# Performance work log

Measured on AMD Instinct MI355X. Metric: run time of the kernel, lower is better.

Reference implementation:

```python
import jax, jax.numpy as jnp
import numpy as np

TAU = 0.1
LAM = 1.0
LOG_NOISE = 1e-12
COS_EPS = 1e-8      # torch CosineSimilarity eps
NORM_EPS = 1e-12    # torch F.normalize eps


def setup_inputs() -> dict:
    key = jax.random.key(0)
    k1, k2, k3, k4 = jax.random.split(key, 4)
    B, D, S = 8192, 128, 64
    z1s = jax.random.normal(k1, (B, D), dtype=jnp.float32)
    z2s = jax.random.normal(k2, (B, D), dtype=jnp.float32)
    z1_c_outs = jax.random.uniform(k3, (B, S), dtype=jnp.float32)
    z1_subject_labels = jax.random.normal(k4, (B, S), dtype=jnp.float32)
    return {"z1s": z1s, "z2s": z2s, "z1_c_outs": z1_c_outs,
            "z1_subject_labels": z1_subject_labels}


def _l2_normalize(x, eps):
    # normalize rows; clamp norm from below like torch
    n = jnp.linalg.norm(x, axis=1, keepdims=True)
    return x / jnp.maximum(n, eps)


def reference(z1s, z2s, z1_c_outs, z1_subject_labels):
    B = z1s.shape[0]
    z1 = z1s.reshape(B, -1)
    z2 = z2s.reshape(B, -1)
    n1 = _l2_normalize(z1, COS_EPS)
    n2 = _l2_normalize(z2, COS_EPS)

    # all-pairs cosine similarities, scaled by temperature
    S12 = jnp.matmul(n1, n2.T) / TAU   # [B, B] sim(z1_i, z2_k)/tau
    S11 = jnp.matmul(n1, n1.T) / TAU   # [B, B] sim(z1_i, z1_k)/tau

    e12 = jnp.exp(S12)
    e11 = jnp.exp(S11)
    numerator = jnp.diagonal(e12)                       # exp(sim(z1_i, z2_i)/tau)
    # denom_i = sum_k e12[i,k] + sum_{k != i} e11[i,k]
    denom = e12.sum(axis=1) + e11.sum(axis=1) - jnp.diagonal(e11)
    contrastive = -jnp.log(LOG_NOISE + numerator / denom)
    loss = contrastive.sum() / (B * (2.0 * B - 1.0))

    # adversarial term: -lam * log(1 - normalized_pred[i, argmax(label_i)])
    c = _l2_normalize(z1_c_outs, NORM_EPS)
    j = jnp.argmax(z1_subject_labels, axis=1)           # [B] int
    picked = c[jnp.arange(B), j]
    loss = loss + LAM * (-jnp.log(LOG_NOISE + 1.0 - picked)).sum()
    return loss
```

## Files before the change

kernel.cpp:

```cpp
#include <hip/hip_runtime.h>
#include <hip/hip_bf16.h>
#include <math.h>


#define NROWS 8192
#define DFEAT 128

typedef __bf16 bf16_t;
typedef __bf16 bf16x8 __attribute__((ext_vector_type(8)));
typedef __bf16 bf16x2 __attribute__((ext_vector_type(2)));
typedef float  f32x4  __attribute__((ext_vector_type(4)));

__device__ __forceinline__ float fexp2(float x) {
#if __has_builtin(__builtin_amdgcn_exp2f)
  return __builtin_amdgcn_exp2f(x);
#else
  return exp2f(x);
#endif
}

__device__ __forceinline__ void stage16(const void* gsrc, void* ldst) {
  __builtin_amdgcn_global_load_lds(
      (const __attribute__((address_space(1))) unsigned int*)gsrc,
      (__attribute__((address_space(3))) unsigned int*)ldst, 16, 0, 0);
}

__global__ __launch_bounds__(256)
void sa_prep_kernel(const float* __restrict__ z1,
                    const float* __restrict__ z2,
                    bf16_t* __restrict__ Abuf,
                    bf16_t* __restrict__ Kc,
                    float* __restrict__ numv,
                    float* __restrict__ d11v) {
  __shared__ __align__(16) bf16_t L[3][16][136];

  int wave = threadIdx.x >> 6;
  int lane = threadIdx.x & 63;
  int tile = blockIdx.x;

  const float SCL = 14.426950408889634f;

#pragma unroll
  for (int r = 0; r < 4; ++r) {
    int rl  = wave * 4 + r;
    int row = tile * 16 + rl;

    float2 a = ((const float2*)(z1 + (size_t)row * DFEAT))[lane];
    float2 b = ((const float2*)(z2 + (size_t)row * DFEAT))[lane];

    float s1  = a.x * a.x + a.y * a.y;
    float s2  = b.x * b.x + b.y * b.y;
    float s12 = a.x * b.x + a.y * b.y;
#pragma unroll
    for (int m = 32; m; m >>= 1) {
      s1  += __shfl_xor(s1, m, 64);
      s2  += __shfl_xor(s2, m, 64);
      s12 += __shfl_xor(s12, m, 64);
    }
    float r1 = 1.0f / fmaxf(sqrtf(s1), 1e-8f);
    float r2 = 1.0f / fmaxf(sqrtf(s2), 1e-8f);

    bf16x2 av;  av[0] = (bf16_t)(a.x * r1 * SCL); av[1] = (bf16_t)(a.y * r1 * SCL);
    bf16x2 k2v; k2v[0] = (bf16_t)(b.x * r2);      k2v[1] = (bf16_t)(b.y * r2);
    bf16x2 k1v; k1v[0] = (bf16_t)(a.x * r1);      k1v[1] = (bf16_t)(a.y * r1);

    *(bf16x2*)&L[0][rl][2 * lane] = av;
    *(bf16x2*)&L[1][rl][2 * lane] = k2v;
    *(bf16x2*)&L[2][rl][2 * lane] = k1v;

    if (lane == 0) {
      numv[row] = expf(10.0f * s12 * r1 * r2);
      d11v[row] = expf(10.0f * s1 * r1 * r1);
    }
  }
  __syncthreads();

#pragma unroll
  for (int sel = 0; sel < 3; ++sel) {
    int u   = threadIdx.x;
    int kf  = u >> 6;
    int qk  = (u >> 4) & 3;
    int r16 = u & 15;
    bf16x8 v = *(const bf16x8*)&L[sel][r16][kf * 32 + qk * 8];
    bf16_t* dst = (sel == 0) ? (Abuf + (size_t)tile * 2048)
                : (sel == 1) ? (Kc + (size_t)tile * 2048)
                             : (Kc + (size_t)(512 + tile) * 2048);
    *(bf16x8*)(dst + u * 8) = v;
  }
}

__global__ __launch_bounds__(512, 4)
void sa_main_kernel(const bf16_t* __restrict__ Abuf,
                    const bf16_t* __restrict__ Kc,
                    float* __restrict__ T2t) {
  __shared__ __align__(16) bf16_t bsm[32768];

  int wave = threadIdx.x >> 6;
  int lane = threadIdx.x & 63;
  int quad = lane >> 4;

  int id     = blockIdx.x;
  int xcd    = id & 7;
  int within = id >> 3;
  int by     = xcd * 8 + (within >> 4);
  int bx     = within & 15;
  int rowBase = bx * 512 + wave * 64;

  const bf16x8* ap = (const bf16x8*)Abuf + (size_t)(rowBase >> 4) * 256 + lane;
  bf16x8 afrag[4][4];
#pragma unroll
  for (int s = 0; s < 4; ++s)
#pragma unroll
    for (int kfi = 0; kfi < 4; ++kfi)
      afrag[s][kfi] = ap[(s * 4 + kfi) * 64];

  const char* src = (const char*)Kc + (size_t)by * 65536 +
                    (size_t)wave * 8192 + (size_t)lane * 16;
  char* dst = (char*)&bsm[0] + wave * 8192;
#pragma unroll
  for (int i = 0; i < 8; ++i) stage16(src + i * 1024, dst + i * 1024);

  __syncthreads();

  f32x4 sums[4];
#pragma unroll
  for (int s = 0; s < 4; ++s) sums[s] = (f32x4){0.f, 0.f, 0.f, 0.f};

#pragma unroll 1
  for (int i = 0; i < 8; ++i) {
    int p = (wave + i) & 7;
    const bf16_t* base = &bsm[0] + p * 4096;
#pragma unroll
    for (int tt = 0; tt < 2; ++tt) {
      const bf16x8* bs = (const bf16x8*)(base + tt * 2048);
      bf16x8 bfr[4];
#pragma unroll
      for (int kfi = 0; kfi < 4; ++kfi) bfr[kfi] = bs[kfi * 64 + lane];
#pragma unroll
      for (int s = 0; s < 4; ++s) {
        f32x4 c = {0.f, 0.f, 0.f, 0.f};
        __builtin_amdgcn_s_setprio(1);
#pragma unroll
        for (int kfi = 0; kfi < 4; ++kfi)
          c = __builtin_amdgcn_mfma_f32_16x16x32_bf16(afrag[s][kfi], bfr[kfi],
                                                      c, 0, 0, 0);
        __builtin_amdgcn_s_setprio(0);
#pragma unroll
        for (int r = 0; r < 4; ++r) sums[s][r] += fexp2(c[r]);
      }
    }
  }

  int l15 = lane & 15;
#pragma unroll
  for (int s = 0; s < 4; ++s) {
    f32x4 st;
#pragma unroll
    for (int r = 0; r < 4; ++r) {
      float v = sums[s][r];
      v += __shfl_xor(v, 1, 64);
      v += __shfl_xor(v, 2, 64);
      v += __shfl_xor(v, 4, 64);
      v += __shfl_xor(v, 8, 64);
      st[r] = v;
    }
    if (l15 == 0)
      *(f32x4*)(T2t + (size_t)by * 8192 + rowBase + s * 16 + quad * 4) = st;
  }
}

__global__ __launch_bounds__(256)
void sa_final_adv_kernel(const float* __restrict__ T2t,
                         const float* __restrict__ numv,
                         const float* __restrict__ d11v,
                         const float* __restrict__ c,
                         const float* __restrict__ lab,
                         float* __restrict__ partial) {
  int wave = threadIdx.x >> 6;
  int lane = threadIdx.x & 63;

  float acc = 0.0f;
#pragma unroll
  for (int i = 0; i < 4; ++i) {
    int row = blockIdx.x * 16 + wave * 4 + i;

    float cv = c[row * 64 + lane];
    float lv = lab[row * 64 + lane];
    float tv = T2t[(size_t)lane * 8192 + row];

    float ss = cv * cv;
    float bestv = lv;
    int   besti = lane;
#pragma unroll
    for (int m = 32; m; m >>= 1) {
      ss += __shfl_xor(ss, m, 64);
      tv += __shfl_xor(tv, m, 64);
      float ov = __shfl_xor(bestv, m, 64);
      int   oi = __shfl_xor(besti, m, 64);
      if (ov > bestv || (ov == bestv && oi < besti)) { bestv = ov; besti = oi; }
    }
    float picked = __shfl(cv, besti, 64) / fmaxf(sqrtf(ss), 1e-12f);

    if (lane == 0) {
      float denom = tv - d11v[row];
      acc += -logf(1e-12f + numv[row] / denom) * (1.0f / 134209536.0f)
             - logf(1e-12f + 1.0f - picked);
    }
  }

  __shared__ float wacc[4];
  if (lane == 0) wacc[wave] = acc;
  __syncthreads();
  if (threadIdx.x == 0)
    partial[blockIdx.x] = wacc[0] + wacc[1] + wacc[2] + wacc[3];
}

__global__ __launch_bounds__(256)
void sa_reduce_kernel(const float* __restrict__ partial,
                      float* __restrict__ out) {
  float v = partial[threadIdx.x] + partial[threadIdx.x + 256];
#pragma unroll
  for (int m = 32; m; m >>= 1) v += __shfl_xor(v, m, 64);
  __shared__ float wacc[4];
  if ((threadIdx.x & 63) == 0) wacc[threadIdx.x >> 6] = v;
  __syncthreads();
  if (threadIdx.x == 0) out[0] = wacc[0] + wacc[1] + wacc[2] + wacc[3];
}

extern "C" void kernel_launch(void* const* d_in, const int* in_sizes, int n_in,
                              void* d_out, int out_size, void* d_ws,
                              size_t ws_size, hipStream_t stream) {
  const float* z1  = (const float*)d_in[0];
  const float* z2  = (const float*)d_in[1];
  const float* co  = (const float*)d_in[2];
  const float* lab = (const float*)d_in[3];
  float* out = (float*)d_out;

  char* ws = (char*)d_ws;
  bf16_t* Abuf  = (bf16_t*)ws;
  bf16_t* Kc    = (bf16_t*)(ws + 2u * 1024 * 1024);
  float*  T2t   = (float*)(ws + 6u * 1024 * 1024);
  float*  numv  = (float*)(ws + 8u * 1024 * 1024);
  float*  d11v  = numv + NROWS;
  float*  part  = d11v + NROWS;

  sa_prep_kernel<<<NROWS / 16, 256, 0, stream>>>(z1, z2, Abuf, Kc, numv,
                                                 d11v);
  sa_main_kernel<<<1024, 512, 0, stream>>>(Abuf, Kc, T2t);
  sa_final_adv_kernel<<<NROWS / 16, 256, 0, stream>>>(T2t, numv, d11v, co,
                                                      lab, part);
  sa_reduce_kernel<<<1, 256, 0, stream>>>(part, out);
}
```

Measured before the change: 108.1 us.

## Exploit symmetry of self-similarity matrix to skip half of e11 tiles

The main kernel now computes only the lower-triangular blocks of the symmetric z1·z1ᵀ exp matrix. Each such block's column sums are accumulated in shared memory and written out as the row sums of the mirrored block, which cuts the grid from 1024 to 784 blocks. This removes roughly a quarter of the MFMA and exp work, at the cost of extra shuffles, LDS accumulation, a barrier and a serial triangle-index search per block.

```diff
diff --git a/kernel.cpp b/kernel.cpp
--- a/kernel.cpp
+++ b/kernel.cpp
@@ -94,17 +94,30 @@
                     const bf16_t* __restrict__ Kc,
                     float* __restrict__ T2t) {
   __shared__ __align__(16) bf16_t bsm[32768];
+  __shared__ float colred[8][256];
 
   int wave = threadIdx.x >> 6;
   int lane = threadIdx.x & 63;
   int quad = lane >> 4;
 
-  int id     = blockIdx.x;
-  int xcd    = id & 7;
-  int within = id >> 3;
-  int by     = xcd * 8 + (within >> 4);
-  int bx     = within & 15;
-  int rowBase = bx * 512 + wave * 64;
+  int id  = blockIdx.x;
+  int swz = (id & 7) * 98 + (id >> 3);
+
+  int I, J, chunk;
+  bool e11;
+  if (swz < 512) {
+    I = swz >> 5; J = swz & 31; chunk = J; e11 = false;
+  } else {
+    int m = swz - 512;
+    I = 0;
+    while ((I + 1) * (I + 2) <= m) ++I;
+    J = m - I * (I + 1);
+    chunk = 32 + J; e11 = true;
+  }
+
+  int rowBase = I * 512 + wave * 64;
+  int aTile   = rowBase >> 8;
+  bool alive  = !e11 || (aTile >= J);
 
   const bf16x8* ap = (const bf16x8*)Abuf + (size_t)(rowBase >> 4) * 256 + lane;
   bf16x8 afrag[4][4];
@@ -114,11 +127,13 @@
     for (int kfi = 0; kfi < 4; ++kfi)
       afrag[s][kfi] = ap[(s * 4 + kfi) * 64];
 
-  const char* src = (const char*)Kc + (size_t)by * 65536 +
+  const char* src = (const char*)Kc + (size_t)chunk * 65536 +
                     (size_t)wave * 8192 + (size_t)lane * 16;
   char* dst = (char*)&bsm[0] + wave * 8192;
 #pragma unroll
   for (int i = 0; i < 8; ++i) stage16(src + i * 1024, dst + i * 1024);
+
+  *(f32x4*)&colred[wave][lane * 4] = (f32x4){0.f, 0.f, 0.f, 0.f};
 
   __syncthreads();
 
@@ -136,6 +151,7 @@
       bf16x8 bfr[4];
 #pragma unroll
       for (int kfi = 0; kfi < 4; ++kfi) bfr[kfi] = bs[kfi * 64 + lane];
+      float cs = 0.0f;
 #pragma unroll
       for (int s = 0; s < 4; ++s) {
         f32x4 c = {0.f, 0.f, 0.f, 0.f};
@@ -145,27 +161,52 @@
           c = __builtin_amdgcn_mfma_f32_16x16x32_bf16(afrag[s][kfi], bfr[kfi],
                                                       c, 0, 0, 0);
         __builtin_amdgcn_s_setprio(0);
-#pragma unroll
-        for (int r = 0; r < 4; ++r) sums[s][r] += fexp2(c[r]);
+        float e0 = fexp2(c[0]), e1 = fexp2(c[1]);
+        float e2 = fexp2(c[2]), e3 = fexp2(c[3]);
+        sums[s][0] += e0; sums[s][1] += e1;
+        sums[s][2] += e2; sums[s][3] += e3;
+        cs += (e0 + e1) + (e2 + e3);
       }
+      if (e11) {
+        cs += __shfl_xor(cs, 16, 64);
+        cs += __shfl_xor(cs, 32, 64);
+        if (lane < 16)
+          colred[wave][p * 32 + tt * 16 + lane] += cs;
+      }
     }
   }
 
   int l15 = lane & 15;
-#pragma unroll
-  for (int s = 0; s < 4; ++s) {
-    f32x4 st;
-#pragma unroll
-    for (int r = 0; r < 4; ++r) {
-      float v = sums[s][r];
-      v += __shfl_xor(v, 1, 64);
-      v += __shfl_xor(v, 2, 64);
-      v += __shfl_xor(v, 4, 64);
-      v += __shfl_xor(v, 8, 64);
-      st[r] = v;
-    }
-    if (l15 == 0)
-      *(f32x4*)(T2t + (size_t)by * 8192 + rowBase + s * 16 + quad * 4) = st;
+  if (alive) {
+#pragma unroll
+    for (int s = 0; s < 4; ++s) {
+      f32x4 st;
+#pragma unroll
+      for (int r = 0; r < 4; ++r) {
+        float v = sums[s][r];
+        v += __shfl_xor(v, 1, 64);
+        v += __shfl_xor(v, 2, 64);
+        v += __shfl_xor(v, 4, 64);
+        v += __shfl_xor(v, 8, 64);
+        st[r] = v;
+      }
+      if (l15 == 0)
+        *(f32x4*)(T2t + (size_t)chunk * 8192 + rowBase + s * 16 + quad * 4) =
+            st;
+    }
+  }
+
+  __syncthreads();
+  if (e11) {
+    int t  = threadIdx.x;
+    int g  = t >> 8;
+    int cc = t & 255;
+    int a  = 2 * I + g;
+    if (a > J) {
+      float v = colred[g * 4 + 0][cc] + colred[g * 4 + 1][cc] +
+                colred[g * 4 + 2][cc] + colred[g * 4 + 3][cc];
+      T2t[(size_t)(32 + a) * 8192 + J * 256 + cc] = v;
+    }
   }
 }
 
@@ -246,7 +287,7 @@
 
   sa_prep_kernel<<<NROWS / 16, 256, 0, stream>>>(z1, z2, Abuf, Kc, numv,
                                                  d11v);
-  sa_main_kernel<<<1024, 512, 0, stream>>>(Abuf, Kc, T2t);
+  sa_main_kernel<<<784, 512, 0, stream>>>(Abuf, Kc, T2t);
   sa_final_adv_kernel<<<NROWS / 16, 256, 0, stream>>>(T2t, numv, d11v, co,
                                                       lab, part);
   sa_reduce_kernel<<<1, 256, 0, stream>>>(part, out);
```

After: 123.7 us. 14.4% more time.
